# Performance work log

Measured on AMD Instinct MI355X. Metric: run time of the kernel, lower is better.

## Reference

```python
import jax, jax.numpy as jnp
import numpy as np

T, HID, H = 1024, 2048, 16
LQ, LKV = 1536, 512
DR, DN, DQ, DV = 64, 128, 192, 128
HI, DI, TOPK = 16, 128, 256
EPS = 1e-6
NEG = -1e30


def _rms(x, g, eps=EPS):
    return x * jax.lax.rsqrt(jnp.mean(x * x, -1, keepdims=True) + eps) * g


def _ln(x, w, b, eps=1e-6):
    m = jnp.mean(x, -1, keepdims=True)
    v = jnp.mean((x - m) ** 2, -1, keepdims=True)
    return (x - m) * jax.lax.rsqrt(v + eps) * w + b


def _rope_interleave(x, cos, sin):
    # HF apply_rotary_pos_emb_interleave: de-interleave even/odd then standard rotate_half.
    x1, x2 = x[..., 0::2], x[..., 1::2]
    xr = jnp.concatenate([x1, x2], -1)
    rot = jnp.concatenate([-x2, x1], -1)
    return xr * cos + rot * sin


def _sparse_indices(hidden, q_lat, cos, sin, ks, ke, i_wqb, i_wk, i_ln_w, i_ln_b, i_wproj):
    # hidden [T,HID], q_lat [T,LQ]; returns [T,TOPK] int32 (sentinel index = T)
    t = hidden.shape[0]
    q_idx = (q_lat @ i_wqb.T).reshape(t, HI, DI)
    k_idx = _ln(hidden @ i_wk.T, i_ln_w, i_ln_b)          # [T,DI]
    w = hidden @ i_wproj.T                                 # [T,HI]
    q_pe = _rope_interleave(q_idx[..., :DR], cos[:, None, :], sin[:, None, :])
    k_pe = _rope_interleave(k_idx[..., :DR], cos, sin)
    qi = jnp.concatenate([q_pe, q_idx[..., DR:]], -1)      # [T,HI,DI]
    ki = jnp.concatenate([k_pe, k_idx[..., DR:]], -1)      # [T,DI]
    weight_scale = DI ** -0.5 * HI ** -0.5
    logits = jnp.einsum('thd,sd->ths', qi, ki)             # [T,HI,T]
    score = jnp.einsum('ths,th->ts', jax.nn.relu(logits), w) * weight_scale
    pos = jnp.arange(t)
    valid = (pos[None, :] >= ks[:, None]) & (pos[None, :] <= ke[:, None])
    score = jnp.where(valid, score, NEG)
    vals, idx = jax.lax.top_k(score, TOPK)
    return jnp.where(vals <= NEG / 2, t, idx).astype(jnp.int32)


def reference(hidden_states, cos, sin, ks, ke,
              w_qa, g_qa, w_qb, w_kva, g_kva, w_kvb, w_o,
              i_wqb, i_wk, i_ln_w, i_ln_b, i_wproj):
    t = hidden_states.shape[1]
    # low-rank projections
    q_lat = _rms(hidden_states @ w_qa.T, g_qa)             # [1,T,LQ]
    ckv = hidden_states @ w_kva.T                          # [1,T,LKV+DR]
    k_c = _rms(ckv[..., :LKV], g_kva)                      # [1,T,LKV]
    k_r = _rope_interleave(ckv[..., LKV:], cos[None], sin[None])  # [1,T,DR]
    # fp8 indexer (reference math in fp32), no-grad in original
    indices = _sparse_indices(hidden_states[0], q_lat[0], cos, sin, ks, ke,
                              i_wqb, i_wk, i_ln_w, i_ln_b, i_wproj)  # [T,TOPK]
    # MLA up-proj with weight absorption
    q_full = (q_lat @ w_qb.T).reshape(1, t, H, DQ)
    q_nope, q_rope = q_full[..., :DN], q_full[..., DN:]
    q_rope = _rope_interleave(q_rope, cos[None, :, None, :], sin[None, :, None, :])
    w_b = w_kvb.reshape(H, DN + DV, LKV)
    w_kn, w_v = w_b[:, :DN, :], w_b[:, DN:, :]
    q_abs = jnp.einsum('bshd,hdk->bshk', q_nope, w_kn)     # absorb k_nope up-proj
    sq = jnp.concatenate([q_abs, q_rope], -1)[0]           # [T,H,LKV+DR]
    skv = jnp.concatenate([k_c, k_r], -1)[0]               # [T,LKV+DR]
    skv = jnp.concatenate([skv, jnp.zeros((1, LKV + DR), skv.dtype)], 0)  # sentinel row
    # sparse attention over gathered top-k KV rows
    kv_g = skv[indices]                                    # [T,TOPK,LKV+DR]
    logits = jnp.einsum('thd,tjd->thj', sq, kv_g) * (DQ ** -0.5)
    logits = jnp.where(indices[:, None, :] == t, NEG, logits)
    p = jax.nn.softmax(logits, -1)
    out = jnp.einsum('thj,tjk->thk', p, kv_g[..., :LKV])   # values = compressed kv
    o = jnp.einsum('thk,hdk->thd', out, w_v)               # un-absorb v up-proj
    return o.reshape(1, t, H * DV) @ w_o.T


def setup_inputs() -> dict:
    key = jax.random.key(0)
    k = jax.random.split(key, 12)
    n = lambda kk, shape, s: jax.random.normal(kk, shape, jnp.float32) * s
    pos = jnp.arange(T, dtype=jnp.float32)
    inv = 1.0 / (10000.0 ** (jnp.arange(0, DR, 2, dtype=jnp.float32) / DR))
    ang = pos[:, None] * inv[None, :]
    cos = jnp.concatenate([jnp.cos(ang), jnp.cos(ang)], -1)
    sin = jnp.concatenate([jnp.sin(ang), jnp.sin(ang)], -1)
    return dict(
        hidden_states=n(k[0], (1, T, HID), 1.0),
        cos=cos, sin=sin,
        ks=jnp.zeros((T,), jnp.int32),
        ke=jnp.arange(T, dtype=jnp.int32),  # causal: keys s <= t valid
        w_qa=n(k[1], (LQ, HID), HID ** -0.5),
        g_qa=jnp.ones((LQ,), jnp.float32),
        w_qb=n(k[2], (H * DQ, LQ), LQ ** -0.5),
        w_kva=n(k[3], (LKV + DR, HID), HID ** -0.5),
        g_kva=jnp.ones((LKV,), jnp.float32),
        w_kvb=n(k[4], (H * (DN + DV), LKV), LKV ** -0.5),
        w_o=n(k[5], (HID, H * DV), (H * DV) ** -0.5),
        i_wqb=n(k[6], (HI * DI, LQ), LQ ** -0.5),
        i_wk=n(k[7], (DI, HID), HID ** -0.5),
        i_ln_w=jnp.ones((DI,), jnp.float32),
        i_ln_b=jnp.zeros((DI,), jnp.float32),
        i_wproj=n(k[8], (HI, HID), HID ** -0.5),
    )
```

## Files before the change

### kernel.cpp

```cpp
#include <hip/hip_runtime.h>
#include <hip/hip_bf16.h>
#include <cmath>

#define T_ 1024
#define HID_ 2048
#define H_ 16
#define LQ_ 1536
#define LKV_ 512
#define DR_ 64
#define DN_ 128
#define DQ_ 192
#define DV_ 128
#define HI_ 16
#define DI_ 128
#define TOPK_ 256
#define NEGF (-1e30f)

typedef short bfrag_t __attribute__((ext_vector_type(8)));
typedef float f32x4 __attribute__((ext_vector_type(4)));

__device__ __forceinline__ float wave_sum64(float v) {
#pragma unroll
  for (int off = 32; off; off >>= 1) v += __shfl_xor(v, off);
  return v;
}

#define GLL(g, l) __builtin_amdgcn_global_load_lds((const __attribute__((address_space(1))) void*)(g), \
                                     (__attribute__((address_space(3))) void*)(l), 16, 0, 0)

__global__ __launch_bounds__(256) void zero_k(float4* __restrict__ p, int n4) {
  int i = blockIdx.x * 256 + threadIdx.x;
  if (i < n4) p[i] = make_float4(0.f, 0.f, 0.f, 0.f);
}

template<typename CT>
__global__ __launch_bounds__(256) void gemm_bf_k(
    const short* __restrict__ A, int lda, long long sA,
    const short* __restrict__ B, int ldb, long long sB,
    CT* __restrict__ C, int ldc, long long sC,
    int Nout, int K)
{
  __shared__ short As[2][128 * 32];
  __shared__ short Bs[2][128 * 32];
  A += (long long)blockIdx.z * sA;
  B += (long long)blockIdx.z * sB;
  C += (long long)blockIdx.z * sC;
  const int tid = threadIdx.x;
  const int bm = blockIdx.y * 128, bn = blockIdx.x * 128;
  const int wave = tid >> 6, lane = tid & 63;
  const int wm = (wave >> 1) * 64, wn = (wave & 1) * 64;
  const int sr = tid >> 2;
  const int scol = (tid & 3) * 8;
  const int m0 = lane & 15, koff = (lane >> 4) * 8;
  f32x4 acc[4][4] = {};
  const short* ga = A + (long long)(bm + sr) * lda + scol;
  const short* gb = B + (long long)(bn + sr) * ldb + scol;
#define STAGE_BF(buf, off) \
    GLL(ga + (off), As[buf] + tid * 8); GLL(ga + (off) + 64 * lda, As[buf] + tid * 8 + 2048); \
    GLL(gb + (off), Bs[buf] + tid * 8); GLL(gb + (off) + 64 * ldb, Bs[buf] + tid * 8 + 2048);
  const int niter = K >> 5;
  STAGE_BF(0, 0);
  for (int it = 0; it < niter; ++it) {
    const int cur = it & 1;
    if (it + 1 < niter) {
      STAGE_BF(cur ^ 1, (it + 1) * 32);
      asm volatile("s_waitcnt vmcnt(4)\ns_barrier" ::: "memory");
    } else {
      asm volatile("s_waitcnt vmcnt(0)\ns_barrier" ::: "memory");
    }
    bfrag_t af[4], bfv[4];
#pragma unroll
    for (int i = 0; i < 4; ++i)
      af[i] = *(const bfrag_t*)(As[cur] + (wm + i * 16 + m0) * 32 + koff);
#pragma unroll
    for (int j = 0; j < 4; ++j)
      bfv[j] = *(const bfrag_t*)(Bs[cur] + (wn + j * 16 + m0) * 32 + koff);
#pragma unroll
    for (int i = 0; i < 4; ++i)
#pragma unroll
      for (int j = 0; j < 4; ++j)
        acc[i][j] = __builtin_amdgcn_mfma_f32_16x16x32_bf16(af[i], bfv[j], acc[i][j], 0, 0, 0);
    asm volatile("s_barrier" ::: "memory");
  }
#undef STAGE_BF
  const int cr = (lane >> 4) * 4, cc = lane & 15;
#pragma unroll
  for (int i = 0; i < 4; ++i) {
    int row = bm + wm + i * 16 + cr;
#pragma unroll
    for (int j = 0; j < 4; ++j) {
      int col = bn + wn + j * 16 + cc;
      if (col < Nout) {
#pragma unroll
        for (int r = 0; r < 4; ++r)
          C[(long long)(row + r) * ldc + col] = (CT)(acc[i][j][r]);
      }
    }
  }
}

__global__ __launch_bounds__(256) void gemm_bfs_k(
    const short* __restrict__ A, int lda,
    const short* __restrict__ B, int ldb,
    float* __restrict__ C, int ldc, int Nout, int K)
{
  __shared__ short As[2][128 * 32];
  __shared__ short Bs[2][128 * 32];
  const long long kbase = (long long)blockIdx.z * K;
  const int tid = threadIdx.x;
  const int bm = blockIdx.y * 128, bn = blockIdx.x * 128;
  const int wave = tid >> 6, lane = tid & 63;
  const int wm = (wave >> 1) * 64, wn = (wave & 1) * 64;
  const int sr = tid >> 2;
  const int scol = (tid & 3) * 8;
  const int m0 = lane & 15, koff = (lane >> 4) * 8;
  f32x4 acc[4][4] = {};
  const short* ga = A + (long long)(bm + sr) * lda + kbase + scol;
  const short* gb = B + (long long)(bn + sr) * ldb + kbase + scol;
#define STAGE_BS(buf, off) \
    GLL(ga + (off), As[buf] + tid * 8); GLL(ga + (off) + 64 * lda, As[buf] + tid * 8 + 2048); \
    GLL(gb + (off), Bs[buf] + tid * 8); GLL(gb + (off) + 64 * ldb, Bs[buf] + tid * 8 + 2048);
  const int niter = K >> 5;
  STAGE_BS(0, 0);
  for (int it = 0; it < niter; ++it) {
    const int cur = it & 1;
    if (it + 1 < niter) {
      STAGE_BS(cur ^ 1, (it + 1) * 32);
      asm volatile("s_waitcnt vmcnt(4)\ns_barrier" ::: "memory");
    } else {
      asm volatile("s_waitcnt vmcnt(0)\ns_barrier" ::: "memory");
    }
    bfrag_t af[4], bfv[4];
#pragma unroll
    for (int i = 0; i < 4; ++i)
      af[i] = *(const bfrag_t*)(As[cur] + (wm + i * 16 + m0) * 32 + koff);
#pragma unroll
    for (int j = 0; j < 4; ++j)
      bfv[j] = *(const bfrag_t*)(Bs[cur] + (wn + j * 16 + m0) * 32 + koff);
#pragma unroll
    for (int i = 0; i < 4; ++i)
#pragma unroll
      for (int j = 0; j < 4; ++j)
        acc[i][j] = __builtin_amdgcn_mfma_f32_16x16x32_bf16(af[i], bfv[j], acc[i][j], 0, 0, 0);
    asm volatile("s_barrier" ::: "memory");
  }
#undef STAGE_BS
  const int cr = (lane >> 4) * 4, cc = lane & 15;
#pragma unroll
  for (int i = 0; i < 4; ++i) {
    int row = bm + wm + i * 16 + cr;
#pragma unroll
    for (int j = 0; j < 4; ++j) {
      int col = bn + wn + j * 16 + cc;
      if (col < Nout) {
#pragma unroll
        for (int r = 0; r < 4; ++r)
          atomicAdd(&C[(long long)(row + r) * ldc + col], acc[i][j][r]);
      }
    }
  }
}

__global__ __launch_bounds__(256) void gemm3_k(
    const short* __restrict__ Ah, const short* __restrict__ Al, int lda,
    const short* __restrict__ Bh, const short* __restrict__ Bl, int ldb,
    float* __restrict__ C, int ldc, int Nout, int K)
{
  __shared__ short Ahs[2][128 * 32];
  __shared__ short Als[2][128 * 32];
  __shared__ short Bhs[2][128 * 32];
  __shared__ short Bls[2][128 * 32];
  const long long kbase = (long long)blockIdx.z * K;
  const int tid = threadIdx.x;
  const int bm = blockIdx.y * 128, bn = blockIdx.x * 128;
  const int wave = tid >> 6, lane = tid & 63;
  const int wm = (wave >> 1) * 64, wn = (wave & 1) * 64;
  const int sr = tid >> 2;
  const int scol = (tid & 3) * 8;
  const int m0 = lane & 15, koff = (lane >> 4) * 8;
  f32x4 acc[4][4] = {};
  const short* gah = Ah + (long long)(bm + sr) * lda + kbase + scol;
  const short* gal = Al + (long long)(bm + sr) * lda + kbase + scol;
  const short* gbh = Bh + (long long)(bn + sr) * ldb + kbase + scol;
  const short* gbl = Bl + (long long)(bn + sr) * ldb + kbase + scol;
#define STAGE_3(buf, off) \
    GLL(gah + (off), Ahs[buf] + tid * 8); GLL(gah + (off) + 64 * lda, Ahs[buf] + tid * 8 + 2048); \
    GLL(gal + (off), Als[buf] + tid * 8); GLL(gal + (off) + 64 * lda, Als[buf] + tid * 8 + 2048); \
    GLL(gbh + (off), Bhs[buf] + tid * 8); GLL(gbh + (off) + 64 * ldb, Bhs[buf] + tid * 8 + 2048); \
    GLL(gbl + (off), Bls[buf] + tid * 8); GLL(gbl + (off) + 64 * ldb, Bls[buf] + tid * 8 + 2048);
  const int niter = K >> 5;
  STAGE_3(0, 0);
  for (int it = 0; it < niter; ++it) {
    const int cur = it & 1;
    if (it + 1 < niter) {
      STAGE_3(cur ^ 1, (it + 1) * 32);
      asm volatile("s_waitcnt vmcnt(8)\ns_barrier" ::: "memory");
    } else {
      asm volatile("s_waitcnt vmcnt(0)\ns_barrier" ::: "memory");
    }
    bfrag_t afh[4], afl[4], bfh[4], bfl[4];
#pragma unroll
    for (int i = 0; i < 4; ++i) {
      afh[i] = *(const bfrag_t*)(Ahs[cur] + (wm + i * 16 + m0) * 32 + koff);
      afl[i] = *(const bfrag_t*)(Als[cur] + (wm + i * 16 + m0) * 32 + koff);
    }
#pragma unroll
    for (int j = 0; j < 4; ++j) {
      bfh[j] = *(const bfrag_t*)(Bhs[cur] + (wn + j * 16 + m0) * 32 + koff);
      bfl[j] = *(const bfrag_t*)(Bls[cur] + (wn + j * 16 + m0) * 32 + koff);
    }
#pragma unroll
    for (int i = 0; i < 4; ++i)
#pragma unroll
      for (int j = 0; j < 4; ++j)
        acc[i][j] = __builtin_amdgcn_mfma_f32_16x16x32_bf16(afh[i], bfh[j], acc[i][j], 0, 0, 0);
#pragma unroll
    for (int i = 0; i < 4; ++i)
#pragma unroll
      for (int j = 0; j < 4; ++j)
        acc[i][j] = __builtin_amdgcn_mfma_f32_16x16x32_bf16(afh[i], bfl[j], acc[i][j], 0, 0, 0);
#pragma unroll
    for (int i = 0; i < 4; ++i)
#pragma unroll
      for (int j = 0; j < 4; ++j)
        acc[i][j] = __builtin_amdgcn_mfma_f32_16x16x32_bf16(afl[i], bfh[j], acc[i][j], 0, 0, 0);
    asm volatile("s_barrier" ::: "memory");
  }
#undef STAGE_3
  const int cr = (lane >> 4) * 4, cc = lane & 15;
  const bool spl = (gridDim.z > 1);
#pragma unroll
  for (int i = 0; i < 4; ++i) {
    int row = bm + wm + i * 16 + cr;
#pragma unroll
    for (int j = 0; j < 4; ++j) {
      int col = bn + wn + j * 16 + cc;
      if (col < Nout) {
#pragma unroll
        for (int r = 0; r < 4; ++r) {
          if (spl) atomicAdd(&C[(long long)(row + r) * ldc + col], acc[i][j][r]);
          else     C[(long long)(row + r) * ldc + col] = acc[i][j][r];
        }
      }
    }
  }
}

__global__ __launch_bounds__(256) void cast_bf16_k(const float* __restrict__ src,
                                                   __hip_bfloat16* __restrict__ dst, int n4) {
  int i = blockIdx.x * 256 + threadIdx.x;
  if (i >= n4) return;
  float4 v = ((const float4*)src)[i];
  union { ushort4 u; __hip_bfloat16 h[4]; } o;
  o.h[0] = __float2bfloat16(v.x); o.h[1] = __float2bfloat16(v.y);
  o.h[2] = __float2bfloat16(v.z); o.h[3] = __float2bfloat16(v.w);
  ((ushort4*)dst)[i] = o.u;
}

__global__ __launch_bounds__(256) void decomp_k(const float* __restrict__ src,
                                                __hip_bfloat16* __restrict__ hi,
                                                __hip_bfloat16* __restrict__ lo, int n4) {
  int i = blockIdx.x * 256 + threadIdx.x;
  if (i >= n4) return;
  float4 v = ((const float4*)src)[i];
  float f[4] = {v.x, v.y, v.z, v.w};
  union { ushort4 u; __hip_bfloat16 h[4]; } oh, ol;
#pragma unroll
  for (int j = 0; j < 4; ++j) {
    __hip_bfloat16 h = __float2bfloat16(f[j]);
    oh.h[j] = h;
    ol.h[j] = __float2bfloat16(f[j] - __bfloat162float(h));
  }
  ((ushort4*)hi)[i] = oh.u;
  ((ushort4*)lo)[i] = ol.u;
}

__global__ __launch_bounds__(256) void cast_pad_k(const float* __restrict__ src,
                                                  __hip_bfloat16* __restrict__ dst,
                                                  int N, int K4, int Npad) {
  int i = blockIdx.x * 256 + threadIdx.x;
  if (i >= Npad * K4) return;
  int r = i / K4;
  float4 v = make_float4(0.f, 0.f, 0.f, 0.f);
  if (r < N) v = ((const float4*)src)[i];
  union { ushort4 u; __hip_bfloat16 h[4]; } o;
  o.h[0] = __float2bfloat16(v.x); o.h[1] = __float2bfloat16(v.y);
  o.h[2] = __float2bfloat16(v.z); o.h[3] = __float2bfloat16(v.w);
  ((ushort4*)dst)[i] = o.u;
}

__global__ __launch_bounds__(256) void wkn_t_k(const float* __restrict__ wkvb,
                                               __hip_bfloat16* __restrict__ dst) {
  __shared__ float tile[64][65];
  const int h = blockIdx.z, k0 = blockIdx.y * 64, d0 = blockIdx.x * 64;
  const int c = threadIdx.x & 63, r0 = threadIdx.x >> 6;
#pragma unroll
  for (int rr = 0; rr < 16; ++rr) {
    int r = r0 + rr * 4;
    tile[r][c] = wkvb[((h * 256 + d0 + r) << 9) + k0 + c];
  }
  __syncthreads();
#pragma unroll
  for (int rr = 0; rr < 16; ++rr) {
    int r = r0 + rr * 4;
    dst[((h * 512 + k0 + r) << 7) + d0 + c] = __float2bfloat16(tile[c][r]);
  }
}

__global__ __launch_bounds__(256) void wv_cast_k(const float* __restrict__ wkvb,
                                                 __hip_bfloat16* __restrict__ dst) {
  int i = blockIdx.x * 256 + threadIdx.x;
  int k = i & 511, dv = (i >> 9) & 127, h = i >> 16;
  dst[i] = __float2bfloat16(wkvb[((h * 256 + 128 + dv) << 9) + k]);
}

__global__ __launch_bounds__(256) void rms_inplace_k(float* x, const float* __restrict__ g,
                                                     int C) {
  int t = blockIdx.x, tid = threadIdx.x;
  float* row = x + (long long)t * C;
  float ss = 0.f;
  for (int i = tid; i < C; i += 256) { float v = row[i]; ss += v * v; }
  __shared__ float red[4];
  ss = wave_sum64(ss);
  if ((tid & 63) == 0) red[tid >> 6] = ss;
  __syncthreads();
  float sc = rsqrtf((red[0] + red[1] + red[2] + red[3]) / (float)C + 1e-6f);
  for (int i = tid; i < C; i += 256) row[i] = row[i] * sc * g[i];
}

__global__ __launch_bounds__(256) void skv_build_k(const float* __restrict__ ckv,
                                                   const float* __restrict__ g,
                                                   const float* __restrict__ cosb,
                                                   const float* __restrict__ sinb,
                                                   __hip_bfloat16* __restrict__ skv) {
  int t = blockIdx.x, tid = threadIdx.x;
  __hip_bfloat16* out = skv + (long long)t * 576;
  if (t == T_) { for (int i = tid; i < 576; i += 256) out[i] = __float2bfloat16(0.f); return; }
  const float* row = ckv + (long long)t * 576;
  float ss = 0.f;
  for (int i = tid; i < 512; i += 256) { float v = row[i]; ss += v * v; }
  __shared__ float red[4];
  ss = wave_sum64(ss);
  if ((tid & 63) == 0) red[tid >> 6] = ss;
  __syncthreads();
  float sc = rsqrtf((red[0] + red[1] + red[2] + red[3]) / 512.f + 1e-6f);
  for (int i = tid; i < 512; i += 256) out[i] = __float2bfloat16(row[i] * sc * g[i]);
  if (tid < 64) {
    int j = tid, j2 = tid & 31;
    float c = cosb[t * 64 + j], s = sinb[t * 64 + j];
    float a = row[512 + 2 * j2], b = row[512 + 2 * j2 + 1];
    out[512 + j] = __float2bfloat16((j < 32) ? (a * c - b * s) : (a * s + b * c));
  }
}

__global__ __launch_bounds__(64) void rope_qi_k(float* qi, const float* __restrict__ cosb,
                                                const float* __restrict__ sinb) {
  int b = blockIdx.x, t = b >> 4, j = threadIdx.x, j2 = j & 31;
  float* x = qi + (long long)b * DI_;
  float c = cosb[t * 64 + j], s = sinb[t * 64 + j];
  float a = x[2 * j2], bb = x[2 * j2 + 1];
  float o = (j < 32) ? (a * c - bb * s) : (a * s + bb * c);
  x[j] = o;
}

__global__ __launch_bounds__(128) void ki_ln_rope_k(float* kbuf, const float* __restrict__ w,
                                                    const float* __restrict__ bia,
                                                    const float* __restrict__ cosb,
                                                    const float* __restrict__ sinb) {
  int t = blockIdx.x, i = threadIdx.x;
  float* row = kbuf + (long long)t * DI_;
  float x = row[i];
  __shared__ float red[2];
  float s1 = wave_sum64(x);
  if ((i & 63) == 0) red[i >> 6] = s1;
  __syncthreads();
  float mean = (red[0] + red[1]) / 128.f;
  float d = x - mean;
  __syncthreads();
  float s2 = wave_sum64(d * d);
  if ((i & 63) == 0) red[i >> 6] = s2;
  __syncthreads();
  float var = (red[0] + red[1]) / 128.f;
  float y = d * rsqrtf(var + 1e-6f) * w[i] + bia[i];
  __shared__ float rowl[128];
  rowl[i] = y;
  __syncthreads();
  float outv = y;
  if (i < 64) {
    int j2 = i & 31;
    float c = cosb[t * 64 + i], s = sinb[t * 64 + i];
    float a = rowl[2 * j2], b = rowl[2 * j2 + 1];
    outv = (i < 32) ? (a * c - b * s) : (a * s + b * c);
  }
  row[i] = outv;
}

__global__ __launch_bounds__(64) void rope_q_sq_k(const __hip_bfloat16* __restrict__ qfull,
                                                  const float* __restrict__ cosb,
                                                  const float* __restrict__ sinb,
                                                  __hip_bfloat16* __restrict__ sq) {
  int b = blockIdx.x, t = b >> 4, h = b & 15, j = threadIdx.x, j2 = j & 31;
  const __hip_bfloat16* x = qfull + (long long)t * 3072 + h * 192 + 128;
  float c = cosb[t * 64 + j], s = sinb[t * 64 + j];
  float a = __bfloat162float(x[2 * j2]), bb = __bfloat162float(x[2 * j2 + 1]);
  float o = (j < 32) ? (a * c - bb * s) : (a * s + bb * c);
  sq[((long long)t * H_ + h) * 576 + 512 + j] = __float2bfloat16(o);
}

__global__ __launch_bounds__(256) void wproj_k(const float* __restrict__ hidden,
                                               const float* __restrict__ wp,
                                               float* __restrict__ out) {
  int wave = threadIdx.x >> 6, lane = threadIdx.x & 63;
  int t = blockIdx.x * 4 + wave;
  const float4* x4 = (const float4*)(hidden + (long long)t * 2048);
  float acc[16] = {};
  for (int c = lane; c < 512; c += 64) {
    float4 xv = x4[c];
#pragma unroll
    for (int h = 0; h < 16; ++h) {
      float4 wv = ((const float4*)(wp + h * 2048))[c];
      acc[h] += xv.x * wv.x + xv.y * wv.y + xv.z * wv.z + xv.w * wv.w;
    }
  }
#pragma unroll
  for (int h = 0; h < 16; ++h) {
    float s = wave_sum64(acc[h]);
    if (lane == 0) out[t * 16 + h] = s;
  }
}

__global__ __launch_bounds__(256) void score_topk_k(
    const short* __restrict__ qi_hi, const short* __restrict__ qi_lo,
    const short* __restrict__ ki_hi, const short* __restrict__ ki_lo,
    const float* __restrict__ wproj, const int* __restrict__ ks,
    const int* __restrict__ ke, int* __restrict__ indices)
{
  __shared__ float s_score[T_];
  __shared__ unsigned s_key[T_];
  __shared__ unsigned s_hist[256];
  __shared__ float s_w[HI_];
  __shared__ unsigned s_wsum[4];
  __shared__ unsigned s_binsel[2];
  __shared__ unsigned s_cnt;
  const int t = blockIdx.x, tid = threadIdx.x;
  const int wave = tid >> 6, lane = tid & 63;
  const int m0 = lane & 15, quad = lane >> 4;
  if (tid < HI_) s_w[tid] = wproj[t * HI_ + tid] * 0.022097086912079608f;
  if (tid == 0) s_cnt = 0;
  __syncthreads();

  bfrag_t ah[4], al[4];
  {
    const short* qh = qi_hi + ((long long)t * HI_ + m0) * DI_ + quad * 8;
    const short* ql = qi_lo + ((long long)t * HI_ + m0) * DI_ + quad * 8;
#pragma unroll
    for (int k = 0; k < 4; ++k) {
      ah[k] = *(const bfrag_t*)(qh + k * 32);
      al[k] = *(const bfrag_t*)(ql + k * 32);
    }
  }
  const int lo = ks[t], hi = ke[t];
  for (int tt = 0; tt < 16; ++tt) {
    const int n0 = wave * 256 + tt * 16;
    const short* kh = ki_hi + (n0 + m0) * DI_ + quad * 8;
    const short* kl = ki_lo + (n0 + m0) * DI_ + quad * 8;
    f32x4 acc = {0.f, 0.f, 0.f, 0.f};
#pragma unroll
    for (int k = 0; k < 4; ++k) {
      bfrag_t bh = *(const bfrag_t*)(kh + k * 32);
      bfrag_t bl = *(const bfrag_t*)(kl + k * 32);
      acc = __builtin_amdgcn_mfma_f32_16x16x32_bf16(ah[k], bh, acc, 0, 0, 0);
      acc = __builtin_amdgcn_mfma_f32_16x16x32_bf16(ah[k], bl, acc, 0, 0, 0);
      acc = __builtin_amdgcn_mfma_f32_16x16x32_bf16(al[k], bh, acc, 0, 0, 0);
    }
    float sc = 0.f;
#pragma unroll
    for (int r = 0; r < 4; ++r) sc += fmaxf(acc[r], 0.f) * s_w[quad * 4 + r];
    sc += __shfl_xor(sc, 16);
    sc += __shfl_xor(sc, 32);
    if (quad == 0) {
      int key = n0 + m0;
      s_score[key] = (key >= lo && key <= hi) ? sc : NEGF;
    }
  }
  __syncthreads();

  const int i0 = tid * 4;
#pragma unroll
  for (int j = 0; j < 4; ++j) {
    unsigned u = __float_as_uint(s_score[i0 + j]);
    s_key[i0 + j] = (u & 0x80000000u) ? ~u : (u | 0x80000000u);
  }
  __syncthreads();

  unsigned prefix = 0, Gprev = 0;
  for (int lvl = 0; lvl < 4; ++lvl) {
    const int shift = 24 - 8 * lvl;
    s_hist[tid] = 0;
    __syncthreads();
#pragma unroll
    for (int j = 0; j < 4; ++j) {
      unsigned k = s_key[i0 + j];
      if (lvl == 0 || (k >> (shift + 8)) == prefix)
        atomicAdd(&s_hist[(k >> shift) & 255u], 1u);
    }
    __syncthreads();
    unsigned h = s_hist[255 - tid];
    unsigned sc_ = h;
    for (int off = 1; off < 64; off <<= 1) {
      unsigned v = __shfl_up(sc_, off);
      if (lane >= off) sc_ += v;
    }
    if (lane == 63) s_wsum[wave] = sc_;
    __syncthreads();
    unsigned wo = 0;
    for (int w = 0; w < wave; ++w) wo += s_wsum[w];
    unsigned incl = sc_ + wo, excl = incl - h;
    unsigned Rn = 256 - Gprev;
    if (excl < Rn && Rn <= incl) { s_binsel[0] = 255 - (unsigned)tid; s_binsel[1] = excl; }
    __syncthreads();
    prefix = (prefix << 8) | s_binsel[0];
    Gprev += s_binsel[1];
  }
  const unsigned thr = prefix;
  const unsigned Rq = 256 - Gprev;
  const unsigned negfkey = ~__float_as_uint(NEGF);

  unsigned eqc = 0;
#pragma unroll
  for (int j = 0; j < 4; ++j) eqc += (s_key[i0 + j] == thr) ? 1u : 0u;
  unsigned esc = eqc;
  for (int off = 1; off < 64; off <<= 1) {
    unsigned v = __shfl_up(esc, off);
    if (lane >= off) esc += v;
  }
  if (lane == 63) s_wsum[wave] = esc;
  __syncthreads();
  unsigned eo = 0;
  for (int w = 0; w < wave; ++w) eo += s_wsum[w];
  unsigned rank = esc + eo - eqc;

#pragma unroll
  for (int j = 0; j < 4; ++j) {
    unsigned k = s_key[i0 + j];
    int outv = (k == negfkey) ? T_ : (i0 + j);
    if (k > thr) {
      unsigned slot = atomicAdd(&s_cnt, 1u);
      indices[t * TOPK_ + slot] = outv;
    } else if (k == thr) {
      if (rank < Rq) indices[t * TOPK_ + Gprev + rank] = outv;
      rank++;
    }
  }
}

#define SP_LD 257
#define PB_LD 264
#define VT_LD 264
__global__ __launch_bounds__(512) void attn_k(
    const short* __restrict__ sq, const short* __restrict__ skv,
    const int* __restrict__ indices, __hip_bfloat16* __restrict__ attn_out)
{
  __shared__ int s_ind[TOPK_];
  __shared__ __align__(16) char s_un[2 * 64 * VT_LD * 2];
  float* s_p  = (float*)s_un;
  short* s_pb = (short*)(s_un + 16448);
  short* s_vt = (short*)s_un;
  const int t = blockIdx.x, tid = threadIdx.x;
  const int wave = tid >> 6, lane = tid & 63;
  const int m0 = lane & 15, quad = lane >> 4;
  if (tid < TOPK_) s_ind[tid] = indices[t * TOPK_ + tid];
  __syncthreads();

  {
    const int jb = wave * 32;
    int rows[2];
    const short* kvp[2];
#pragma unroll
    for (int j = 0; j < 2; ++j) {
      rows[j] = s_ind[jb + j * 16 + m0];
      kvp[j] = skv + rows[j] * 576 + quad * 8;
    }
    const short* qp = sq + ((long long)t * H_ + m0) * 576 + quad * 8;
    f32x4 qacc[2] = {};
    for (int ks = 0; ks < 18; ++ks) {
      const int k0 = ks * 32;
      bfrag_t aq = *(const bfrag_t*)(qp + k0);
#pragma unroll
      for (int j = 0; j < 2; ++j) {
        bfrag_t bq = *(const bfrag_t*)(kvp[j] + k0);
        qacc[j] = __builtin_amdgcn_mfma_f32_16x16x32_bf16(aq, bq, qacc[j], 0, 0, 0);
      }
    }
    const float scale = 0.07216878364870322f;
#pragma unroll
    for (int j = 0; j < 2; ++j) {
      int key = jb + j * 16 + m0;
      bool msk = (rows[j] == T_);
#pragma unroll
      for (int r = 0; r < 4; ++r)
        s_p[(quad * 4 + r) * SP_LD + key] = msk ? NEGF : qacc[j][r] * scale;
    }
  }
  __syncthreads();

  for (int h = wave * 2; h < wave * 2 + 2; ++h) {
    float* ph = s_p + h * SP_LD;
    float m = -3.4e38f;
    for (int j = lane; j < TOPK_; j += 64) m = fmaxf(m, ph[j]);
#pragma unroll
    for (int off = 32; off; off >>= 1) m = fmaxf(m, __shfl_xor(m, off));
    float sum = 0.f;
    for (int j = lane; j < TOPK_; j += 64) {
      float e = __expf(ph[j] - m);
      ph[j] = e; sum += e;
    }
    sum = wave_sum64(sum);
    float inv = 1.f / sum;
    for (int j = lane; j < TOPK_; j += 64) ph[j] *= inv;
  }
  __syncthreads();

  {
    const int col = tid & 255, h0 = tid >> 8;
#pragma unroll
    for (int h = 0; h < 8; ++h) {
      const int hh = h0 + h * 2;
      s_pb[hh * PB_LD + col] =
          (short)__bfloat16_as_ushort(__float2bfloat16(s_p[hh * SP_LD + col]));
    }
  }
  __syncthreads();

  bfrag_t apf[8];
#pragma unroll
  for (int kk = 0; kk < 8; ++kk)
    apf[kk] = *(const bfrag_t*)(s_pb + m0 * PB_LD + kk * 32 + quad * 8);

  const int grp = wave >> 2, gw = wave & 3;
  short* svt = s_vt + grp * (64 * VT_LD);
  const int r8 = (tid >> 3) & 31;
  const int bb = tid & 7;

  for (int cc = 0; cc < 4; ++cc) {
    const int c = grp * 4 + cc;
    __syncthreads();
#pragma unroll
    for (int rep = 0; rep < 8; ++rep) {
      const int kv = r8 + 32 * rep;
      const int row = s_ind[kv];
      bfrag_t v = *(const bfrag_t*)(skv + (long long)row * 576 + c * 64 + bb * 8);
      const int colx = kv ^ (bb << 3);
#pragma unroll
      for (int j = 0; j < 8; ++j)
        svt[(bb * 8 + j) * VT_LD + colx] = v[j];
    }
    __syncthreads();
    const int d = gw * 16 + m0;
    const short* vrow = svt + d * VT_LD;
    const int sx = (d >> 3) << 3;
    f32x4 oacc = {0.f, 0.f, 0.f, 0.f};
#pragma unroll
    for (int kk = 0; kk < 8; ++kk) {
      bfrag_t bv = *(const bfrag_t*)(vrow + ((kk * 32 + quad * 8) ^ sx));
      oacc = __builtin_amdgcn_mfma_f32_16x16x32_bf16(apf[kk], bv, oacc, 0, 0, 0);
    }
    const int col = c * 64 + d;
#pragma unroll
    for (int r = 0; r < 4; ++r)
      attn_out[((long long)t * H_ + quad * 4 + r) * 512 + col] = __float2bfloat16(oacc[r]);
  }
}

extern "C" void kernel_launch(void* const* d_in, const int* in_sizes, int n_in,
                              void* d_out, int out_size, void* d_ws, size_t ws_size,
                              hipStream_t stream) {
  const float* hidden  = (const float*)d_in[0];
  const float* cosb    = (const float*)d_in[1];
  const float* sinb    = (const float*)d_in[2];
  const int*   ks      = (const int*)d_in[3];
  const int*   ke      = (const int*)d_in[4];
  const float* w_qa    = (const float*)d_in[5];
  const float* g_qa    = (const float*)d_in[6];
  const float* w_qb    = (const float*)d_in[7];
  const float* w_kva   = (const float*)d_in[8];
  const float* g_kva   = (const float*)d_in[9];
  const float* w_kvb   = (const float*)d_in[10];
  const float* w_o     = (const float*)d_in[11];
  const float* i_wqb   = (const float*)d_in[12];
  const float* i_wk    = (const float*)d_in[13];
  const float* i_ln_w  = (const float*)d_in[14];
  const float* i_ln_b  = (const float*)d_in[15];
  const float* i_wproj = (const float*)d_in[16];
  float* out = (float*)d_out;
  (void)in_sizes; (void)n_in; (void)out_size; (void)ws_size;

  char* ws = (char*)d_ws;
  __hip_bfloat16* hid_hi  = (__hip_bfloat16*)(ws + 0);
  __hip_bfloat16* hid_lo  = (__hip_bfloat16*)(ws + 4194304);
  float*          q_lat   = (float*)(ws + 8388608);
  __hip_bfloat16* qi_hi   = (__hip_bfloat16*)(ws + 8388608);
  __hip_bfloat16* qlat_hi = (__hip_bfloat16*)(ws + 14680064);
  __hip_bfloat16* qlat_lo = (__hip_bfloat16*)(ws + 17825792);
  float*          qi      = (float*)(ws + 20971520);
  float*          kib     = (float*)(ws + 29360128);
  float*          wbuf    = (float*)(ws + 29884416);
  float*          ckv     = (float*)(ws + 29949952);
  __hip_bfloat16* qi_lo   = (__hip_bfloat16*)(ws + 29949952);
  __hip_bfloat16* ki_hi   = (__hip_bfloat16*)(ws + 34144256);
  __hip_bfloat16* ki_lo   = (__hip_bfloat16*)(ws + 34406400);
  __hip_bfloat16* sq_bf   = (__hip_bfloat16*)(ws + 0);
  __hip_bfloat16* o_bf    = (__hip_bfloat16*)(ws + 0);
  __hip_bfloat16* W       = (__hip_bfloat16*)(ws + 37748736);
  __hip_bfloat16* skv_bf  = (__hip_bfloat16*)(ws + 47185920);
  int*            idxb    = (int*)(ws + 48366720);
  __hip_bfloat16* E       = (__hip_bfloat16*)(ws + 49415296);

  dim3 blk(256);
  const short* Ws = (const short*)W;
  const short* Es = (const short*)E;

  decomp_k<<<2048, blk, 0, stream>>>(hidden, hid_hi, hid_lo, 524288);

  decomp_k<<<3072, blk, 0, stream>>>(w_qa, W, E, 786432);
  zero_k<<<1536, blk, 0, stream>>>((float4*)q_lat, 393216);
  gemm3_k<<<dim3(12, 8, 4), blk, 0, stream>>>(
      (const short*)hid_hi, (const short*)hid_lo, HID_, Ws, Es, HID_, q_lat, LQ_, LQ_, 512);
  rms_inplace_k<<<T_, blk, 0, stream>>>(q_lat, g_qa, LQ_);

  cast_pad_k<<<1280, blk, 0, stream>>>(w_kva, W, 576, 512, 640);
  zero_k<<<576, blk, 0, stream>>>((float4*)ckv, 147456);
  gemm_bfs_k<<<dim3(5, 8, 4), blk, 0, stream>>>(
      (const short*)hid_hi, HID_, Ws, HID_, ckv, 576, 576, 512);
  skv_build_k<<<T_ + 1, blk, 0, stream>>>(ckv, g_kva, cosb, sinb, skv_bf);

  decomp_k<<<1536, blk, 0, stream>>>(q_lat, qlat_hi, qlat_lo, 393216);

  decomp_k<<<3072, blk, 0, stream>>>(i_wqb, W, E, 786432);
  zero_k<<<2048, blk, 0, stream>>>((float4*)qi, 524288);
  gemm3_k<<<dim3(16, 8, 4), blk, 0, stream>>>(
      (const short*)qlat_hi, (const short*)qlat_lo, LQ_, Ws, Es, LQ_, qi, HI_ * DI_, HI_ * DI_, 384);
  rope_qi_k<<<T_ * HI_, dim3(64), 0, stream>>>(qi, cosb, sinb);
  decomp_k<<<2048, blk, 0, stream>>>(qi, qi_hi, qi_lo, 524288);

  decomp_k<<<256, blk, 0, stream>>>(i_wk, W, E, 65536);
  zero_k<<<128, blk, 0, stream>>>((float4*)kib, 32768);
  gemm3_k<<<dim3(1, 8, 16), blk, 0, stream>>>(
      (const short*)hid_hi, (const short*)hid_lo, HID_, Ws, Es, HID_, kib, DI_, DI_, 128);
  ki_ln_rope_k<<<T_, dim3(128), 0, stream>>>(kib, i_ln_w, i_ln_b, cosb, sinb);
  decomp_k<<<128, blk, 0, stream>>>(kib, ki_hi, ki_lo, 32768);

  wproj_k<<<256, blk, 0, stream>>>(hidden, i_wproj, wbuf);

  score_topk_k<<<T_, blk, 0, stream>>>(
      (const short*)qi_hi, (const short*)qi_lo, (const short*)ki_hi, (const short*)ki_lo,
      wbuf, ks, ke, idxb);

  cast_bf16_k<<<4608, blk, 0, stream>>>(w_qb, W, 1179648);
  gemm_bf_k<__hip_bfloat16><<<dim3(24, 8, 1), blk, 0, stream>>>(
      (const short*)qlat_hi, LQ_, 0, Ws, LQ_, 0, (__hip_bfloat16*)E, H_ * DQ_, 0, H_ * DQ_, LQ_);
  rope_q_sq_k<<<T_ * H_, dim3(64), 0, stream>>>(E, cosb, sinb, sq_bf);

  wkn_t_k<<<dim3(2, 8, 16), blk, 0, stream>>>(w_kvb, W);
  gemm_bf_k<__hip_bfloat16><<<dim3(4, 8, 16), blk, 0, stream>>>(
      Es, H_ * DQ_, 192, Ws, DI_, 65536, sq_bf, H_ * 576, 576, LKV_, DN_);

  attn_k<<<T_, dim3(512), 0, stream>>>((const short*)sq_bf, (const short*)skv_bf, idxb, E);

  wv_cast_k<<<4096, blk, 0, stream>>>(w_kvb, W);
  gemm_bf_k<__hip_bfloat16><<<dim3(1, 8, 16), blk, 0, stream>>>(
      Es, H_ * LKV_, 512, Ws, LKV_, 65536, o_bf, H_ * DV_, 128, DV_, LKV_);

  cast_bf16_k<<<4096, blk, 0, stream>>>(w_o, W, 1048576);
  zero_k<<<2048, blk, 0, stream>>>((float4*)out, 524288);
  gemm_bfs_k<<<dim3(16, 8, 4), blk, 0, stream>>>(
      (const short*)o_bf, H_ * DV_, Ws, H_ * DV_, out, HID_, HID_, 512);
}
```

Measured before the change: 581.7 us.

## Split indexer scoring from top-k selection and aggregate histogram atomics per wave

The fused score+top-k kernel is split into a score kernel launched on a 4×T grid, which writes scores to global memory, and a separate top-k kernel that reads each row into registers. Key fragments are now loaded before the MFMA chain. The radix histogram and output-slot atomics use ballot-based aggregation across the wave, which reduces LDS atomic contention. The trade-off is an extra global round trip for a T×T score matrix, one more kernel launch, and extra ballot instructions per element.

```diff
diff --git a/kernel.cpp b/kernel.cpp
--- a/kernel.cpp
+++ b/kernel.cpp
@@ -429,69 +429,81 @@
   }
 }
 
-__global__ __launch_bounds__(256) void score_topk_k(
+__global__ __launch_bounds__(256) void score_k(
     const short* __restrict__ qi_hi, const short* __restrict__ qi_lo,
     const short* __restrict__ ki_hi, const short* __restrict__ ki_lo,
     const float* __restrict__ wproj, const int* __restrict__ ks,
-    const int* __restrict__ ke, int* __restrict__ indices)
+    const int* __restrict__ ke, float* __restrict__ scores)
 {
-  __shared__ float s_score[T_];
-  __shared__ unsigned s_key[T_];
+  __shared__ float s_w[HI_];
+  const int seg = blockIdx.x, t = blockIdx.y, tid = threadIdx.x;
+  const int wave = tid >> 6, lane = tid & 63;
+  const int m0 = lane & 15, quad = lane >> 4;
+  if (tid < HI_) s_w[tid] = wproj[t * HI_ + tid] * 0.022097086912079608f;
+  __syncthreads();
+
+  bfrag_t ah[4], al[4];
+  {
+    const short* qh = qi_hi + ((long long)t * HI_ + m0) * DI_ + quad * 8;
+    const short* ql = qi_lo + ((long long)t * HI_ + m0) * DI_ + quad * 8;
+#pragma unroll
+    for (int k = 0; k < 4; ++k) {
+      ah[k] = *(const bfrag_t*)(qh + k * 32);
+      al[k] = *(const bfrag_t*)(ql + k * 32);
+    }
+  }
+  const int lo = ks[t], hi = ke[t];
+  float* srow = scores + t * T_;
+#pragma unroll
+  for (int tt = 0; tt < 4; ++tt) {
+    const int n0 = seg * 256 + wave * 64 + tt * 16;
+    const short* kh = ki_hi + (n0 + m0) * DI_ + quad * 8;
+    const short* kl = ki_lo + (n0 + m0) * DI_ + quad * 8;
+    bfrag_t bh[4], bl[4];
+#pragma unroll
+    for (int k = 0; k < 4; ++k) {
+      bh[k] = *(const bfrag_t*)(kh + k * 32);
+      bl[k] = *(const bfrag_t*)(kl + k * 32);
+    }
+    f32x4 acc = {0.f, 0.f, 0.f, 0.f};
+#pragma unroll
+    for (int k = 0; k < 4; ++k) {
+      acc = __builtin_amdgcn_mfma_f32_16x16x32_bf16(ah[k], bh[k], acc, 0, 0, 0);
+      acc = __builtin_amdgcn_mfma_f32_16x16x32_bf16(ah[k], bl[k], acc, 0, 0, 0);
+      acc = __builtin_amdgcn_mfma_f32_16x16x32_bf16(al[k], bh[k], acc, 0, 0, 0);
+    }
+    float sc = 0.f;
+#pragma unroll
+    for (int r = 0; r < 4; ++r) sc += fmaxf(acc[r], 0.f) * s_w[quad * 4 + r];
+    sc += __shfl_xor(sc, 16);
+    sc += __shfl_xor(sc, 32);
+    if (quad == 0) {
+      int key = n0 + m0;
+      srow[key] = (key >= lo && key <= hi) ? sc : NEGF;
+    }
+  }
+}
+
+__global__ __launch_bounds__(256) void topk_k(const float* __restrict__ scores,
+                                              int* __restrict__ indices)
+{
   __shared__ unsigned s_hist[256];
-  __shared__ float s_w[HI_];
   __shared__ unsigned s_wsum[4];
   __shared__ unsigned s_binsel[2];
   __shared__ unsigned s_cnt;
   const int t = blockIdx.x, tid = threadIdx.x;
   const int wave = tid >> 6, lane = tid & 63;
-  const int m0 = lane & 15, quad = lane >> 4;
-  if (tid < HI_) s_w[tid] = wproj[t * HI_ + tid] * 0.022097086912079608f;
+  const int i0 = tid * 4;
   if (tid == 0) s_cnt = 0;
-  __syncthreads();
-
-  bfrag_t ah[4], al[4];
-  {
-    const short* qh = qi_hi + ((long long)t * HI_ + m0) * DI_ + quad * 8;
-    const short* ql = qi_lo + ((long long)t * HI_ + m0) * DI_ + quad * 8;
-#pragma unroll
-    for (int k = 0; k < 4; ++k) {
-      ah[k] = *(const bfrag_t*)(qh + k * 32);
-      al[k] = *(const bfrag_t*)(ql + k * 32);
-    }
-  }
-  const int lo = ks[t], hi = ke[t];
-  for (int tt = 0; tt < 16; ++tt) {
-    const int n0 = wave * 256 + tt * 16;
-    const short* kh = ki_hi + (n0 + m0) * DI_ + quad * 8;
-    const short* kl = ki_lo + (n0 + m0) * DI_ + quad * 8;
-    f32x4 acc = {0.f, 0.f, 0.f, 0.f};
-#pragma unroll
-    for (int k = 0; k < 4; ++k) {
-      bfrag_t bh = *(const bfrag_t*)(kh + k * 32);
-      bfrag_t bl = *(const bfrag_t*)(kl + k * 32);
-      acc = __builtin_amdgcn_mfma_f32_16x16x32_bf16(ah[k], bh, acc, 0, 0, 0);
-      acc = __builtin_amdgcn_mfma_f32_16x16x32_bf16(ah[k], bl, acc, 0, 0, 0);
-      acc = __builtin_amdgcn_mfma_f32_16x16x32_bf16(al[k], bh, acc, 0, 0, 0);
-    }
-    float sc = 0.f;
-#pragma unroll
-    for (int r = 0; r < 4; ++r) sc += fmaxf(acc[r], 0.f) * s_w[quad * 4 + r];
-    sc += __shfl_xor(sc, 16);
-    sc += __shfl_xor(sc, 32);
-    if (quad == 0) {
-      int key = n0 + m0;
-      s_score[key] = (key >= lo && key <= hi) ? sc : NEGF;
-    }
-  }
-  __syncthreads();
-
-  const int i0 = tid * 4;
+
+  float4 sv = ((const float4*)(scores + t * T_))[tid];
+  float f[4] = {sv.x, sv.y, sv.z, sv.w};
+  unsigned key[4];
 #pragma unroll
   for (int j = 0; j < 4; ++j) {
-    unsigned u = __float_as_uint(s_score[i0 + j]);
-    s_key[i0 + j] = (u & 0x80000000u) ? ~u : (u | 0x80000000u);
-  }
-  __syncthreads();
+    unsigned u = __float_as_uint(f[j]);
+    key[j] = (u & 0x80000000u) ? ~u : (u | 0x80000000u);
+  }
 
   unsigned prefix = 0, Gprev = 0;
   for (int lvl = 0; lvl < 4; ++lvl) {
@@ -500,9 +512,17 @@
     __syncthreads();
 #pragma unroll
     for (int j = 0; j < 4; ++j) {
-      unsigned k = s_key[i0 + j];
-      if (lvl == 0 || (k >> (shift + 8)) == prefix)
-        atomicAdd(&s_hist[(k >> shift) & 255u], 1u);
+      unsigned k = key[j];
+      bool part = (lvl == 0) || ((k >> (shift + 8)) == prefix);
+      unsigned bin = (k >> shift) & 255u;
+      unsigned long long mask = __ballot(part);
+#pragma unroll
+      for (int b = 0; b < 8; ++b) {
+        unsigned long long bal = __ballot((bin >> b) & 1u);
+        mask &= ((bin >> b) & 1u) ? bal : ~bal;
+      }
+      if (part && lane == (__ffsll((long long)mask) - 1))
+        atomicAdd(&s_hist[bin], (unsigned)__popcll(mask));
     }
     __syncthreads();
     unsigned h = s_hist[255 - tid];
@@ -528,7 +548,7 @@
 
   unsigned eqc = 0;
 #pragma unroll
-  for (int j = 0; j < 4; ++j) eqc += (s_key[i0 + j] == thr) ? 1u : 0u;
+  for (int j = 0; j < 4; ++j) eqc += (key[j] == thr) ? 1u : 0u;
   unsigned esc = eqc;
   for (int off = 1; off < 64; off <<= 1) {
     unsigned v = __shfl_up(esc, off);
@@ -542,12 +562,21 @@
 
 #pragma unroll
   for (int j = 0; j < 4; ++j) {
-    unsigned k = s_key[i0 + j];
+    unsigned k = key[j];
     int outv = (k == negfkey) ? T_ : (i0 + j);
-    if (k > thr) {
-      unsigned slot = atomicAdd(&s_cnt, 1u);
-      indices[t * TOPK_ + slot] = outv;
-    } else if (k == thr) {
+    bool gt = (k > thr);
+    unsigned long long bal = __ballot(gt);
+    if (bal) {
+      int leader = __ffsll((long long)bal) - 1;
+      unsigned base = 0;
+      if (lane == leader) base = atomicAdd(&s_cnt, (unsigned)__popcll(bal));
+      base = (unsigned)__shfl((int)base, leader);
+      if (gt) {
+        unsigned pre = (unsigned)__popcll(bal & ((1ull << lane) - 1ull));
+        indices[t * TOPK_ + base + pre] = outv;
+      }
+    }
+    if (!gt && k == thr) {
       if (rank < Rq) indices[t * TOPK_ + Gprev + rank] = outv;
       rank++;
     }
@@ -703,6 +732,7 @@
   __hip_bfloat16* qlat_hi = (__hip_bfloat16*)(ws + 14680064);
   __hip_bfloat16* qlat_lo = (__hip_bfloat16*)(ws + 17825792);
   float*          qi      = (float*)(ws + 20971520);
+  float*          scoresb = (float*)(ws + 20971520);
   float*          kib     = (float*)(ws + 29360128);
   float*          wbuf    = (float*)(ws + 29884416);
   float*          ckv     = (float*)(ws + 29949952);
@@ -752,9 +782,10 @@
 
   wproj_k<<<256, blk, 0, stream>>>(hidden, i_wproj, wbuf);
 
-  score_topk_k<<<T_, blk, 0, stream>>>(
+  score_k<<<dim3(4, T_), blk, 0, stream>>>(
       (const short*)qi_hi, (const short*)qi_lo, (const short*)ki_hi, (const short*)ki_lo,
-      wbuf, ks, ke, idxb);
+      wbuf, ks, ke, scoresb);
+  topk_k<<<T_, blk, 0, stream>>>(scoresb, idxb);
 
   cast_bf16_k<<<4608, blk, 0, stream>>>(w_qb, W, 1179648);
   gemm_bf_k<__hip_bfloat16><<<dim3(24, 8, 1), blk, 0, stream>>>(
```

Result: slower. 594.3 us (+2.2%).
